# Performance work log

Measured on AMD Instinct MI355X. Metric: run time of the kernel, lower is better.

Reference implementation:

```python
import jax, jax.numpy as jnp
import numpy as np

B, T, D, H = 8, 256, 1024, 512
NUM_SPANS = T * (T + 1) // 2          # triangular span enumeration
K = int(2.0 * T)                      # pruning_ratio * num_tokens
NUM_GOLD = 10
NEG = -1e20                           # allennlp replace_masked_values fill

# static triangular (start, end) index tables: for start in range(T): for end in range(start, T)
_starts = np.repeat(np.arange(T), np.arange(T, 0, -1))
_ends = np.concatenate([np.arange(s, T) for s in range(T)])
START_IDX = jnp.asarray(_starts, dtype=jnp.int32)
END_IDX = jnp.asarray(_ends, dtype=jnp.int32)


def setup_inputs() -> dict:
    key = jax.random.key(0)
    ks = jax.random.split(key, 8)
    inputs = jax.random.normal(ks[0], (B, T, D), dtype=jnp.float32)
    input_mask = jnp.ones((B, T), dtype=jnp.int32)
    # gold spans with start <= end, all in range (sorted along last dim)
    answer_spans = jnp.sort(jax.random.randint(ks[1], (B, NUM_GOLD, 2), 0, T), axis=-1)
    sD = 1.0 / np.sqrt(D)
    sH = 1.0 / np.sqrt(H)
    W_start = jax.random.uniform(ks[2], (D, H), jnp.float32, -sD, sD)
    b_start = jax.random.uniform(ks[3], (H,), jnp.float32, -sD, sD)
    W_end = jax.random.uniform(ks[4], (D, H), jnp.float32, -sD, sD)
    b_end = jax.random.uniform(ks[5], (H,), jnp.float32, -sD, sD)
    w_score = jax.random.uniform(ks[6], (H, 1), jnp.float32, -sH, sH)
    b_score = jax.random.uniform(ks[7], (1,), jnp.float32, -sH, sH)
    return {"inputs": inputs, "input_mask": input_mask, "answer_spans": answer_spans,
            "W_start": W_start, "b_start": b_start, "W_end": W_end, "b_end": b_end,
            "w_score": w_score, "b_score": b_score}


def reference(inputs, input_mask, answer_spans, W_start, b_start, W_end, b_end, w_score, b_score):
    # SpanRepAssembly: project starts/ends, pairwise-sum over triangular spans
    hs = inputs @ W_start + b_start                        # [B,T,H]
    he = inputs @ W_end + b_end                            # [B,T,H]
    span_hidden = hs[:, START_IDX, :] + he[:, END_IDX, :]  # [B,S,H]
    m = input_mask.astype(bool)
    span_mask = m[:, START_IDX] & m[:, END_IDX]            # [B,S]

    # span scorer: ReLU -> Linear(H,1)
    scores = jax.nn.relu(span_hidden) @ w_score + b_score  # [B,S,1]
    scores = jnp.where(span_mask[..., None], scores, NEG)

    # Pruner: top-k by score, indices sorted ascending, gather
    _, top_idx = jax.lax.top_k(scores[..., 0], K)          # [B,K]
    top_idx = jnp.sort(top_idx, axis=1)
    top_logits = jnp.take_along_axis(scores, top_idx[..., None], axis=1)       # [B,K,1]
    top_mask = jnp.take_along_axis(span_mask, top_idx, axis=1)[..., None].astype(jnp.float32)
    top_probs = jax.nn.sigmoid(top_logits) * top_mask

    # gold prediction map (union policy): labels[b, tri_index(span)] = 1
    s0 = answer_spans[..., 0].astype(jnp.int32)
    e0 = answer_spans[..., 1].astype(jnp.int32)
    gmask = (s0 >= 0)
    arg_idx = (2 * s0 * T - s0 * s0 + s0) // 2 + (e0 - s0)
    arg_idx = jnp.where(gmask, arg_idx, 0)
    labels = jnp.zeros((B, NUM_SPANS), jnp.float32)
    labels = labels.at[jnp.arange(B)[:, None], arg_idx].max(gmask.astype(jnp.float32))
    pred = jnp.take_along_axis(labels[..., None], top_idx[..., None], axis=1)  # [B,K,1]

    # BCE-with-logits, weight=top_mask, reduction='sum' (stable form)
    l = top_logits
    bce = jnp.maximum(l, 0.0) - l * pred + jnp.log1p(jnp.exp(-jnp.abs(l)))
    loss = jnp.sum(top_mask * bce)
    return top_probs, loss
```

## Files before the change

kernel.cpp:

```cpp
#include <hip/hip_runtime.h>
#include <hip/hip_bf16.h>
#include <math.h>

#define BB 8
#define TT 256
#define DD 1024
#define HH 512
#define NSPANS 32896
#define KK 512
#define NEGV -1e20f
#define NCH 32
#define CHSZ 1028
#define NTILE 136

typedef __attribute__((ext_vector_type(8))) short bf16x8;
typedef __attribute__((ext_vector_type(4))) float f32x4;

__device__ inline unsigned short f2bf(float f) {
    unsigned u = __float_as_uint(f);
    return (unsigned short)((u + 0x7FFFu + ((u >> 16) & 1u)) >> 16);
}
__device__ inline float bf2f(unsigned short u) {
    return __uint_as_float(((unsigned)u) << 16);
}
__device__ inline void split3(float v, unsigned short& a, unsigned short& b,
                              unsigned short& c) {
    a = f2bf(v);           float r  = v - bf2f(a);
    b = f2bf(r);           float r2 = r - bf2f(b);
    c = f2bf(r2);
}

__global__ __launch_bounds__(256) void cvt_x(
    const float* __restrict__ X, unsigned short* __restrict__ x0,
    unsigned short* __restrict__ x1, unsigned short* __restrict__ x2)
{
    const int i4 = blockIdx.x * 256 + threadIdx.x;
    const float4 v = ((const float4*)X)[i4];
    const float vv[4] = {v.x, v.y, v.z, v.w};
    ushort4 h0, h1, h2;
    unsigned short* p0 = (unsigned short*)&h0;
    unsigned short* p1 = (unsigned short*)&h1;
    unsigned short* p2 = (unsigned short*)&h2;
    #pragma unroll
    for (int j = 0; j < 4; ++j) split3(vv[j], p0[j], p1[j], p2[j]);
    ((ushort4*)x0)[i4] = h0;
    ((ushort4*)x1)[i4] = h1;
    ((ushort4*)x2)[i4] = h2;
}

__global__ __launch_bounds__(256) void cvt_w(
    const float* __restrict__ Ws, const float* __restrict__ We,
    unsigned short* __restrict__ wt)
{
    const int idx = blockIdx.x * 256 + threadIdx.x;
    const int z = idx >> 19;
    const int p = idx & 524287;
    const int h = p >> 10, d = p & 1023;
    const float v = (z ? We : Ws)[d * HH + h];
    unsigned short a, b, c;
    split3(v, a, b, c);
    unsigned short* base = wt + (size_t)z * 3 * 524288;
    base[0 * 524288 + p] = a;
    base[1 * 524288 + p] = b;
    base[2 * 524288 + p] = c;
}

__global__ __launch_bounds__(256) void gemm_mfma(
    const unsigned short* __restrict__ xs,
    const unsigned short* __restrict__ wt,
    const float* __restrict__ bs, const float* __restrict__ be,
    float* __restrict__ hs, float* __restrict__ he)
{
    const int bid = blockIdx.x;
    const int lg  = ((bid & 7) << 6) + (bid >> 3);
    const int z   = lg >> 8;
    const int my  = (lg & 255) >> 3, nx = lg & 7;
    const int m0 = my * 64, n0 = nx * 64;

    const unsigned short* __restrict__ W = wt + (size_t)z * 3 * 524288;
    const float* __restrict__ bias = z ? be : bs;
    float* __restrict__ Y = z ? he : hs;

    __shared__ __align__(16) unsigned short la[3][64][72];
    __shared__ __align__(16) unsigned short lb[3][64][72];

    const int tid = threadIdx.x;
    const int wave = tid >> 6, lane = tid & 63;
    const int wm = (wave >> 1) * 32, wn = (wave & 1) * 32;

    f32x4 acc[2][2];
    #pragma unroll
    for (int i = 0; i < 2; ++i)
        #pragma unroll
        for (int j = 0; j < 2; ++j) acc[i][j] = (f32x4){0.f, 0.f, 0.f, 0.f};

    const int rA = lane & 15;
    const int kq = lane >> 4;

    for (int kt = 0; kt < 16; ++kt) {
        const int k0 = kt * 64;
        __syncthreads();
        #pragma unroll
        for (int sp = 0; sp < 3; ++sp) {
            #pragma unroll
            for (int it = 0; it < 2; ++it) {
                const int idx = it * 256 + tid;
                const int row = idx >> 3, c8 = idx & 7;
                *(int4*)&la[sp][row][c8 * 8] =
                    *(const int4*)&xs[(size_t)sp * 2097152 + (m0 + row) * 1024 + k0 + c8 * 8];
                *(int4*)&lb[sp][row][c8 * 8] =
                    *(const int4*)&W[(size_t)sp * 524288 + (n0 + row) * 1024 + k0 + c8 * 8];
            }
        }
        __syncthreads();

        #pragma unroll
        for (int s = 0; s < 2; ++s) {
            const int kl = s * 32 + kq * 8;
            bf16x8 af[3][2], bg[3][2];
            #pragma unroll
            for (int sp = 0; sp < 3; ++sp) {
                #pragma unroll
                for (int f = 0; f < 2; ++f) {
                    af[sp][f] = *(const bf16x8*)&la[sp][wm + f * 16 + rA][kl];
                    bg[sp][f] = *(const bf16x8*)&lb[sp][wn + f * 16 + rA][kl];
                }
            }
            #pragma unroll
            for (int fm = 0; fm < 2; ++fm)
                #pragma unroll
                for (int fn = 0; fn < 2; ++fn) {
                    acc[fm][fn] = __builtin_amdgcn_mfma_f32_16x16x32_bf16(
                        af[0][fm], bg[0][fn], acc[fm][fn], 0, 0, 0);
                    acc[fm][fn] = __builtin_amdgcn_mfma_f32_16x16x32_bf16(
                        af[0][fm], bg[1][fn], acc[fm][fn], 0, 0, 0);
                    acc[fm][fn] = __builtin_amdgcn_mfma_f32_16x16x32_bf16(
                        af[1][fm], bg[0][fn], acc[fm][fn], 0, 0, 0);
                    acc[fm][fn] = __builtin_amdgcn_mfma_f32_16x16x32_bf16(
                        af[1][fm], bg[1][fn], acc[fm][fn], 0, 0, 0);
                    acc[fm][fn] = __builtin_amdgcn_mfma_f32_16x16x32_bf16(
                        af[0][fm], bg[2][fn], acc[fm][fn], 0, 0, 0);
                    acc[fm][fn] = __builtin_amdgcn_mfma_f32_16x16x32_bf16(
                        af[2][fm], bg[0][fn], acc[fm][fn], 0, 0, 0);
                }
        }
    }

    const int col = lane & 15, rq = lane >> 4;
    #pragma unroll
    for (int fm = 0; fm < 2; ++fm)
        #pragma unroll
        for (int fn = 0; fn < 2; ++fn) {
            const int nn = n0 + wn + fn * 16 + col;
            const float bv = bias[nn];
            #pragma unroll
            for (int r = 0; r < 4; ++r) {
                const int mm = m0 + wm + fm * 16 + rq * 4 + r;
                Y[mm * HH + nn] = acc[fm][fn][r] + bv;
            }
        }
}

__device__ inline unsigned f2key(float f) {
    unsigned u = __float_as_uint(f);
    return u ^ ((u & 0x80000000u) ? 0xFFFFFFFFu : 0x80000000u);
}

__global__ __launch_bounds__(256) void span_scores(
    const float* __restrict__ hs, const float* __restrict__ he,
    const float* __restrict__ w_score, const float* __restrict__ b_score,
    const int* __restrict__ input_mask, float* __restrict__ scores,
    unsigned* __restrict__ hist12)
{
    const int bx = blockIdx.x;
    const int b = bx / NTILE;
    int tI = bx - b * NTILE;
    int i = 0, cum = 0;
    while (tI >= cum + (16 - i)) { cum += 16 - i; ++i; }
    const int j = i + (tI - cum);
    const int s0 = i * 16, e0 = j * 16;

    __shared__ float shs[16][516];
    __shared__ float she[16][516];
    __shared__ float sw[512];
    __shared__ unsigned lh[2048];

    const int tid = threadIdx.x;
    const float4* hs4 = (const float4*)hs;
    const float4* he4 = (const float4*)he;

    for (int idx = tid; idx < 2048; idx += 256) lh[idx] = 0;

    for (int idx = tid; idx < 4096; idx += 256) {
        const int row = idx >> 7;
        const int c4  = idx & 127;
        if (row < 16) {
            *(float4*)&shs[row][c4*4] = hs4[((b*TT + s0 + row) * HH) / 4 + c4];
        } else {
            *(float4*)&she[row - 16][c4*4] = he4[((b*TT + e0 + row - 16) * HH) / 4 + c4];
        }
    }
    if (tid < 128) *(float4*)&sw[tid*4] = ((const float4*)w_score)[tid];
    __syncthreads();

    const int ii = tid >> 4, jj = tid & 15;
    const int s = s0 + ii, e = e0 + jj;

    float4 acc4 = make_float4(0.f, 0.f, 0.f, 0.f);
    #pragma unroll 4
    for (int c4 = 0; c4 < 128; ++c4) {
        const float4 a = *(const float4*)&shs[ii][c4*4];
        const float4 v = *(const float4*)&she[jj][c4*4];
        const float4 w = *(const float4*)&sw[c4*4];
        acc4.x += fmaxf(a.x + v.x, 0.f) * w.x;
        acc4.y += fmaxf(a.y + v.y, 0.f) * w.y;
        acc4.z += fmaxf(a.z + v.z, 0.f) * w.z;
        acc4.w += fmaxf(a.w + v.w, 0.f) * w.w;
    }

    if (e >= s) {
        float scv = (acc4.x + acc4.y) + (acc4.z + acc4.w) + b_score[0];
        if (!(input_mask[b*TT + s] && input_mask[b*TT + e])) scv = NEGV;
        scores[b*NSPANS + s*TT - (s*(s-1))/2 + (e - s)] = scv;
        const unsigned bin = f2key(scv) >> 20;
        atomicAdd(&lh[bin >> 1], 1u << ((bin & 1u) * 16));
    }
    __syncthreads();

    for (int idx = tid; idx < 2048; idx += 256) {
        const unsigned w = lh[idx];
        const unsigned lo = w & 0xFFFFu, hi = w >> 16;
        if (lo) atomicAdd(&hist12[b*4096 + 2*idx],     lo);
        if (hi) atomicAdd(&hist12[b*4096 + 2*idx + 1], hi);
    }
}

__global__ __launch_bounds__(1024) void find12(
    const unsigned* __restrict__ hist12, unsigned* __restrict__ thrInfo)
{
    const int b = blockIdx.x;
    const unsigned* h = hist12 + b*4096;
    const int tid = threadIdx.x;
    const int lane = tid & 63, wave = tid >> 6;

    const int hi = 4095 - tid*4;
    unsigned psum = h[hi] + h[hi-1] + h[hi-2] + h[hi-3];

    unsigned inc = psum;
    #pragma unroll
    for (int off = 1; off < 64; off <<= 1) {
        unsigned n = __shfl_up(inc, off);
        if (lane >= off) inc += n;
    }
    __shared__ unsigned wsum[16], wpre[16];
    if (lane == 63) wsum[wave] = inc;
    __syncthreads();
    if (tid == 0) { unsigned c = 0; for (int w = 0; w < 16; ++w) { wpre[w] = c; c += wsum[w]; } }
    __syncthreads();

    const unsigned before = wpre[wave] + inc - psum;
    if (before < KK && before + psum >= KK && psum > 0) {
        unsigned cum = before;
        int bin = hi;
        for (int jj = 0; jj < 4; ++jj) {
            const unsigned c = h[hi - jj];
            if (cum + c >= KK) { bin = hi - jj; break; }
            cum += c;
        }
        thrInfo[b*4 + 0] = (unsigned)bin;
        thrInfo[b*4 + 1] = KK - cum;
    }
}

__global__ __launch_bounds__(256) void compact_cand(
    const float* __restrict__ scores, const unsigned* __restrict__ thrInfo,
    unsigned* __restrict__ cand, unsigned* __restrict__ candCnt)
{
    const int b = blockIdx.x >> 5, ch = blockIdx.x & 31;
    const float* sc = scores + b*NSPANS;
    const unsigned p12 = thrInfo[b*4 + 0];
    const int base = ch*CHSZ;
    for (int i = base + threadIdx.x; i < base + CHSZ; i += 256) {
        const unsigned key = f2key(sc[i]);
        if ((key >> 20) == p12) {
            const unsigned pos = atomicAdd(&candCnt[b], 1u);
            cand[b*NSPANS + pos] = key & 0xFFFFFu;
        }
    }
}

__global__ __launch_bounds__(1024) void refine(
    const unsigned* __restrict__ cand, const unsigned* __restrict__ candCnt,
    const float* __restrict__ scores,
    unsigned* __restrict__ thrInfo, unsigned* __restrict__ chunkBase)
{
    const int b = blockIdx.x;
    const unsigned* cd = cand + b*NSPANS;
    const unsigned n = candCnt[b];
    const unsigned remaining = thrInfo[b*4 + 1];
    const int tid = threadIdx.x;
    const int lane = tid & 63, wave = tid >> 6;

    __shared__ unsigned hist[1024];
    __shared__ unsigned wsum[16], wpre[16];
    __shared__ unsigned sh[2], shT[2];

    hist[tid] = 0;
    __syncthreads();
    for (unsigned i = tid; i < n; i += 1024) atomicAdd(&hist[(cd[i] >> 10) & 1023u], 1u);
    __syncthreads();
    {
        const unsigned psum = hist[1023 - tid];
        unsigned inc = psum;
        #pragma unroll
        for (int off = 1; off < 64; off <<= 1) {
            unsigned v = __shfl_up(inc, off);
            if (lane >= off) inc += v;
        }
        if (lane == 63) wsum[wave] = inc;
        __syncthreads();
        if (tid == 0) { unsigned c = 0; for (int w = 0; w < 16; ++w) { wpre[w] = c; c += wsum[w]; } }
        __syncthreads();
        const unsigned before = wpre[wave] + inc - psum;
        if (before < remaining && before + psum >= remaining && psum > 0) {
            sh[0] = 1023u - (unsigned)tid;
            sh[1] = remaining - before;
        }
        __syncthreads();
    }
    const unsigned b1 = sh[0], rem1 = sh[1];
    __syncthreads();

    hist[tid] = 0;
    __syncthreads();
    for (unsigned i = tid; i < n; i += 1024) {
        const unsigned v = cd[i];
        if (((v >> 10) & 1023u) == b1) atomicAdd(&hist[v & 1023u], 1u);
    }
    __syncthreads();
    {
        const unsigned psum = hist[1023 - tid];
        unsigned inc = psum;
        #pragma unroll
        for (int off = 1; off < 64; off <<= 1) {
            unsigned v = __shfl_up(inc, off);
            if (lane >= off) inc += v;
        }
        if (lane == 63) wsum[wave] = inc;
        __syncthreads();
        if (tid == 0) { unsigned c = 0; for (int w = 0; w < 16; ++w) { wpre[w] = c; c += wsum[w]; } }
        __syncthreads();
        const unsigned before = wpre[wave] + inc - psum;
        if (before < rem1 && before + psum >= rem1 && psum > 0) {
            const unsigned thrv = (thrInfo[b*4 + 0] << 20) | (b1 << 10) | (1023u - (unsigned)tid);
            thrInfo[b*4 + 2] = thrv;
            thrInfo[b*4 + 3] = rem1 - before;
            shT[0] = thrv;
            shT[1] = rem1 - before;
        }
    }
    __syncthreads();
    const unsigned thr = shT[0], ties = shT[1];

    __shared__ unsigned cg[NCH], ce[NCH];
    const float* sc = scores + b*NSPANS;
    #pragma unroll
    for (int q = 0; q < 2; ++q) {
        const int ch = wave*2 + q;
        const int base = ch*CHSZ, end = base + CHSZ;
        unsigned g = 0, e = 0;
        for (int i = base + lane; i < end; i += 64) {
            const unsigned key = f2key(sc[i]);
            g += (key > thr); e += (key == thr);
        }
        #pragma unroll
        for (int off = 32; off; off >>= 1) { g += __shfl_down(g, off); e += __shfl_down(e, off); }
        if (lane == 0) { cg[ch] = g; ce[ch] = e; }
    }
    __syncthreads();

    if (tid == 0) {
        unsigned out = 0, eqp = 0;
        for (int c = 0; c < NCH; ++c) {
            chunkBase[(b*NCH + c)*2 + 0] = out;
            chunkBase[(b*NCH + c)*2 + 1] = eqp;
            const unsigned room = (eqp >= ties) ? 0u : (ties - eqp);
            const unsigned taken = (ce[c] < room) ? ce[c] : room;
            out += cg[c] + taken;
            eqp += ce[c];
        }
    }
}

__global__ __launch_bounds__(256) void scatter(
    const float* __restrict__ scores, const unsigned* __restrict__ thrInfo,
    const unsigned* __restrict__ chunkBase, int* __restrict__ top_idx)
{
    const int b = blockIdx.x >> 5, ch = blockIdx.x & 31;
    const float* sc = scores + b*NSPANS;
    const unsigned thr = thrInfo[b*4 + 2], ties = thrInfo[b*4 + 3];
    unsigned outPos = chunkBase[(b*NCH + ch)*2 + 0];
    unsigned eqPos  = chunkBase[(b*NCH + ch)*2 + 1];

    const int tid = threadIdx.x, wave = tid >> 6, lane = tid & 63;
    const unsigned long long lmask = (1ull << lane) - 1ull;
    __shared__ unsigned wS[4], wE[4];

    const int base = ch*CHSZ;
    for (int seg = base; seg < base + CHSZ; seg += 256) {
        const int i = seg + tid;
        const bool valid = (i < base + CHSZ);
        const unsigned key = valid ? f2key(sc[i]) : 0u;
        const bool g  = valid && key > thr;
        const bool eq = valid && key == thr;

        const unsigned long long meq = __ballot(eq);
        if (lane == 0) wE[wave] = (unsigned)__popcll(meq);
        __syncthreads();

        unsigned eqPre = eqPos;
        for (int w = 0; w < wave; ++w) eqPre += wE[w];
        const unsigned myEqRank = eqPre + (unsigned)__popcll(meq & lmask);
        const bool sel = g || (eq && myEqRank < ties);

        const unsigned long long msel = __ballot(sel);
        if (lane == 0) wS[wave] = (unsigned)__popcll(msel);
        __syncthreads();

        unsigned selPre = outPos;
        for (int w = 0; w < wave; ++w) selPre += wS[w];
        if (sel) top_idx[b*KK + selPre + (unsigned)__popcll(msel & lmask)] = i;

        unsigned totS = 0, totE = 0;
        #pragma unroll
        for (int w = 0; w < 4; ++w) { totS += wS[w]; totE += wE[w]; }
        __syncthreads();
        outPos += totS; eqPos += totE;
    }
}

__global__ __launch_bounds__(1024) void finalize(
    const float* __restrict__ scores, const int* __restrict__ top_idx,
    const int* __restrict__ answer_spans, float* __restrict__ out)
{
    __shared__ int gold[BB*10];
    __shared__ float part[16];
    const int tid = threadIdx.x;

    if (tid < BB*10) {
        const int s0 = answer_spans[tid*2];
        const int e0 = answer_spans[tid*2 + 1];
        gold[tid] = (s0 >= 0) ? ((2*s0*TT - s0*s0 + s0)/2 + (e0 - s0)) : -1;
    }
    __syncthreads();

    float lsum = 0.f;
    for (int t = tid; t < BB*KK; t += 1024) {
        const int b = t >> 9;
        const int idx = top_idx[t];
        const float l = scores[b*NSPANS + idx];
        float prob = 0.f;
        if (l > -1e19f) {
            prob = 1.f / (1.f + expf(-l));
            float pred = 0.f;
            #pragma unroll
            for (int g = 0; g < 10; ++g)
                if (gold[b*10 + g] == idx) pred = 1.f;
            lsum += fmaxf(l, 0.f) - l*pred + log1pf(expf(-fabsf(l)));
        }
        out[t] = prob;
    }

    #pragma unroll
    for (int off = 32; off; off >>= 1) lsum += __shfl_down(lsum, off);
    const int wave = tid >> 6, lane = tid & 63;
    if (lane == 0) part[wave] = lsum;
    __syncthreads();
    if (tid == 0) {
        float ssum = 0.f;
        for (int w = 0; w < 16; ++w) ssum += part[w];
        out[BB*KK] = ssum;
    }
}

extern "C" void kernel_launch(void* const* d_in, const int* in_sizes, int n_in,
                              void* d_out, int out_size, void* d_ws, size_t ws_size,
                              hipStream_t stream)
{
    const float* inputs       = (const float*)d_in[0];
    const int*   input_mask   = (const int*)  d_in[1];
    const int*   answer_spans = (const int*)  d_in[2];
    const float* W_start      = (const float*)d_in[3];
    const float* b_start      = (const float*)d_in[4];
    const float* W_end        = (const float*)d_in[5];
    const float* b_end        = (const float*)d_in[6];
    const float* w_score      = (const float*)d_in[7];
    const float* b_score      = (const float*)d_in[8];
    float* out = (float*)d_out;
    unsigned* ws = (unsigned*)d_ws;

    float*    hs       = (float*)(ws);
    float*    he       = (float*)(ws + 1048576);
    float*    scores   = (float*)(ws + 2097152);
    int*      top_idx  = (int*)  (ws + 2360320);
    unsigned* thrInfo  = ws + 2364416;
    unsigned* chunkBase= ws + 2364448;
    unsigned* hist12   = ws + 2364960;
    unsigned* candCnt  = ws + 2397728;
    unsigned short* xs = (unsigned short*)(ws + 2397736);
    unsigned short* wt = (unsigned short*)(ws + 5543464);
    unsigned* cand     = (unsigned*)hs;

    hipMemsetAsync(hist12, 0, (size_t)(BB*4096 + BB)*4, stream);

    cvt_x<<<2048, 256, 0, stream>>>(inputs, xs, xs + 2097152, xs + 4194304);
    cvt_w<<<4096, 256, 0, stream>>>(W_start, W_end, wt);
    gemm_mfma<<<512, 256, 0, stream>>>(xs, wt, b_start, b_end, hs, he);

    span_scores<<<BB*NTILE, 256, 0, stream>>>(hs, he, w_score, b_score, input_mask,
                                              scores, hist12);

    find12      <<<BB, 1024, 0, stream>>>(hist12, thrInfo);
    compact_cand<<<BB*NCH, 256, 0, stream>>>(scores, thrInfo, cand, candCnt);
    refine      <<<BB, 1024, 0, stream>>>(cand, candCnt, scores, thrInfo, chunkBase);
    scatter     <<<BB*NCH, 256, 0, stream>>>(scores, thrInfo, chunkBase, top_idx);

    finalize<<<1, 1024, 0, stream>>>(scores, top_idx, answer_spans, out);
}
```

Before: 139.2 us.

## Use 32x32 span tiles with 2x2 register blocking and K-chunked LDS staging

The span scoring kernel now covers 32x32 (start,end) tiles instead of 16x16, and each thread computes a 2x2 block of spans. The hidden dimension is staged through shared memory in four 128-wide chunks, so the LDS footprint stays small. Each hs/he row load is reused across more spans, which cuts global and LDS traffic per span. The cost is fewer blocks (288 instead of 1088), which lowers parallelism on a large GPU, plus more wasted work on diagonal tiles and extra barriers per chunk.

```diff
diff --git a/kernel.cpp b/kernel.cpp
--- a/kernel.cpp
+++ b/kernel.cpp
@@ -11,7 +11,7 @@
 #define NEGV -1e20f
 #define NCH 32
 #define CHSZ 1028
-#define NTILE 136
+#define NT32 36
 
 typedef __attribute__((ext_vector_type(8))) short bf16x8;
 typedef __attribute__((ext_vector_type(4))) float f32x4;
@@ -173,16 +173,16 @@
     unsigned* __restrict__ hist12)
 {
     const int bx = blockIdx.x;
-    const int b = bx / NTILE;
-    int tI = bx - b * NTILE;
+    const int b = bx / NT32;
+    int tI = bx - b * NT32;
     int i = 0, cum = 0;
-    while (tI >= cum + (16 - i)) { cum += 16 - i; ++i; }
+    while (tI >= cum + (8 - i)) { cum += 8 - i; ++i; }
     const int j = i + (tI - cum);
-    const int s0 = i * 16, e0 = j * 16;
-
-    __shared__ float shs[16][516];
-    __shared__ float she[16][516];
-    __shared__ float sw[512];
+    const int s0 = i * 32, e0 = j * 32;
+
+    __shared__ __align__(16) float shs[32][132];
+    __shared__ __align__(16) float she[32][132];
+    __shared__ __align__(16) float swc[128];
     __shared__ unsigned lh[2048];
 
     const int tid = threadIdx.x;
@@ -191,39 +191,68 @@
 
     for (int idx = tid; idx < 2048; idx += 256) lh[idx] = 0;
 
-    for (int idx = tid; idx < 4096; idx += 256) {
-        const int row = idx >> 7;
-        const int c4  = idx & 127;
-        if (row < 16) {
-            *(float4*)&shs[row][c4*4] = hs4[((b*TT + s0 + row) * HH) / 4 + c4];
-        } else {
-            *(float4*)&she[row - 16][c4*4] = he4[((b*TT + e0 + row - 16) * HH) / 4 + c4];
-        }
-    }
-    if (tid < 128) *(float4*)&sw[tid*4] = ((const float4*)w_score)[tid];
-    __syncthreads();
-
     const int ii = tid >> 4, jj = tid & 15;
-    const int s = s0 + ii, e = e0 + jj;
-
-    float4 acc4 = make_float4(0.f, 0.f, 0.f, 0.f);
-    #pragma unroll 4
-    for (int c4 = 0; c4 < 128; ++c4) {
-        const float4 a = *(const float4*)&shs[ii][c4*4];
-        const float4 v = *(const float4*)&she[jj][c4*4];
-        const float4 w = *(const float4*)&sw[c4*4];
-        acc4.x += fmaxf(a.x + v.x, 0.f) * w.x;
-        acc4.y += fmaxf(a.y + v.y, 0.f) * w.y;
-        acc4.z += fmaxf(a.z + v.z, 0.f) * w.z;
-        acc4.w += fmaxf(a.w + v.w, 0.f) * w.w;
-    }
-
-    if (e >= s) {
-        float scv = (acc4.x + acc4.y) + (acc4.z + acc4.w) + b_score[0];
-        if (!(input_mask[b*TT + s] && input_mask[b*TT + e])) scv = NEGV;
-        scores[b*NSPANS + s*TT - (s*(s-1))/2 + (e - s)] = scv;
-        const unsigned bin = f2key(scv) >> 20;
-        atomicAdd(&lh[bin >> 1], 1u << ((bin & 1u) * 16));
+
+    float4 acc[2][2];
+    #pragma unroll
+    for (int p = 0; p < 2; ++p)
+        #pragma unroll
+        for (int q = 0; q < 2; ++q) acc[p][q] = make_float4(0.f, 0.f, 0.f, 0.f);
+
+    for (int ck = 0; ck < 4; ++ck) {
+        const int kc = ck * 128;
+        __syncthreads();
+        #pragma unroll
+        for (int l = 0; l < 4; ++l) {
+            const int idx = l * 256 + tid;
+            const int row = idx >> 5, c4 = idx & 31;
+            *(float4*)&shs[row][c4 * 4] =
+                hs4[((b*TT + s0 + row) * HH + kc) / 4 + c4];
+            *(float4*)&she[row][c4 * 4] =
+                he4[((b*TT + e0 + row) * HH + kc) / 4 + c4];
+        }
+        if (tid < 32) *(float4*)&swc[tid * 4] =
+            ((const float4*)w_score)[kc / 4 + tid];
+        __syncthreads();
+
+        #pragma unroll 4
+        for (int c4 = 0; c4 < 32; ++c4) {
+            const float4 w  = *(const float4*)&swc[c4 * 4];
+            const float4 a0 = *(const float4*)&shs[ii][c4 * 4];
+            const float4 a1 = *(const float4*)&shs[ii + 16][c4 * 4];
+            const float4 v0 = *(const float4*)&she[jj][c4 * 4];
+            const float4 v1 = *(const float4*)&she[jj + 16][c4 * 4];
+            #pragma unroll
+            for (int p = 0; p < 2; ++p) {
+                const float4 a = p ? a1 : a0;
+                #pragma unroll
+                for (int q = 0; q < 2; ++q) {
+                    const float4 v = q ? v1 : v0;
+                    acc[p][q].x += fmaxf(a.x + v.x, 0.f) * w.x;
+                    acc[p][q].y += fmaxf(a.y + v.y, 0.f) * w.y;
+                    acc[p][q].z += fmaxf(a.z + v.z, 0.f) * w.z;
+                    acc[p][q].w += fmaxf(a.w + v.w, 0.f) * w.w;
+                }
+            }
+        }
+    }
+
+    const float bsc = b_score[0];
+    #pragma unroll
+    for (int p = 0; p < 2; ++p) {
+        const int s = s0 + ii + p * 16;
+        #pragma unroll
+        for (int q = 0; q < 2; ++q) {
+            const int e = e0 + jj + q * 16;
+            if (e >= s) {
+                const float4 a4 = acc[p][q];
+                float scv = (a4.x + a4.y) + (a4.z + a4.w) + bsc;
+                if (!(input_mask[b*TT + s] && input_mask[b*TT + e])) scv = NEGV;
+                scores[b*NSPANS + s*TT - (s*(s-1))/2 + (e - s)] = scv;
+                const unsigned bin = f2key(scv) >> 20;
+                atomicAdd(&lh[bin >> 1], 1u << ((bin & 1u) * 16));
+            }
+        }
     }
     __syncthreads();
 
@@ -517,8 +546,8 @@
     cvt_w<<<4096, 256, 0, stream>>>(W_start, W_end, wt);
     gemm_mfma<<<512, 256, 0, stream>>>(xs, wt, b_start, b_end, hs, he);
 
-    span_scores<<<BB*NTILE, 256, 0, stream>>>(hs, he, w_score, b_score, input_mask,
-                                              scores, hist12);
+    span_scores<<<BB*NT32, 256, 0, stream>>>(hs, he, w_score, b_score, input_mask,
+                                             scores, hist12);
 
     find12      <<<BB, 1024, 0, stream>>>(hist12, thrInfo);
     compact_cand<<<BB*NCH, 256, 0, stream>>>(scores, thrInfo, cand, candCnt);
```

Result: faster. 123.4 us (-11.3%).
